# Kernel tuning notes

Hardware: AMD Instinct MI355X
Metric: run time of the kernel (lower is better)

The kernel has to match this reference:

```python
import jax, jax.numpy as jnp
import numpy as np

SHOT, WAY, DIM, Q, R = 5, 32, 640, 4096, 10
TEMP, L, DIV = 16.0, 2.0, 10.0
EPS = 1e-5


def _expmap0(x, c):
    # x: (..., d); c: broadcastable to (..., 1). Exponential map at origin + ball projection.
    sc = jnp.sqrt(c)
    n = jnp.maximum(jnp.linalg.norm(x, axis=-1, keepdims=True), EPS)
    y = jnp.tanh(sc * n) * x / (sc * n)
    ny = jnp.maximum(jnp.linalg.norm(y, axis=-1, keepdims=True), EPS)
    maxn = (1.0 - 1e-3) / sc
    return jnp.where(ny > maxn, y * (maxn / ny), y)


def _dist(x, y, c):
    # Poincare distance: 2/sqrt(c) * artanh(sqrt(c) * ||mobius_add(-x, y)||)
    u = -x
    uy = jnp.sum(u * y, -1, keepdims=True)
    u2 = jnp.sum(u * u, -1, keepdims=True)
    y2 = jnp.sum(y * y, -1, keepdims=True)
    num = (1.0 + 2.0 * c * uy + c * y2) * u + (1.0 - c * u2) * y
    den = jnp.maximum(1.0 + 2.0 * c * uy + c * c * u2 * y2, EPS)
    n = jnp.linalg.norm(num / den, axis=-1, keepdims=True)
    sc = jnp.sqrt(c)
    arg = jnp.clip(sc * n, 0.0, 1.0 - EPS)
    return ((2.0 / sc) * jnp.arctanh(arg))[..., 0]


def setup_inputs() -> dict:
    key = jax.random.key(0)
    ks = jax.random.split(key, 8)
    f = lambda k, s: jax.random.normal(k, s, dtype=jnp.float32)
    z = lambda s: jnp.zeros(s, jnp.float32)
    return {
        "data_shot": f(ks[0], (SHOT * WAY, DIM)),
        "data_query": f(ks[1], (Q, DIM)),
        "W1": f(ks[2], (2 * DIM, 128)) * 0.05, "b1": z((128,)),
        "W2": f(ks[3], (128, 64)) * 0.05, "b2": z((64,)),
        "W3": f(ks[4], (64, 5)) * 0.05, "b3": z((5,)),
        "Wr1": f(ks[5], (2 * R + 2, R)) * 0.05, "br1": z((R,)),
        "Wr2": f(ks[6], (R, R + 1)) * 0.05, "br2": z((R + 1,)),
    }


def reference(data_shot, data_query, W1, b1, W2, b2, W3, b3, Wr1, br1, Wr2, br2):
    # --- episode stats + per-class curvature controller ---
    all_data = jnp.concatenate([data_shot, data_query], 0).mean(0)      # (dim,)
    protos = data_shot.reshape(SHOT, WAY, DIM).mean(0)                  # (way, dim)
    ctrl_in = jnp.concatenate([protos, jnp.broadcast_to(all_data, (WAY, DIM))], 1)
    h = jax.nn.relu(ctrl_in @ W1 + b1)
    h = jax.nn.relu(h @ W2 + b2)
    cand = jnp.arange(1, 6, dtype=jnp.float32) * (L / DIV)              # 5 curvature candidates
    c = jax.nn.softmax(h @ W3 + b3, axis=-1) @ cand                     # (way,) positive curvature

    # --- hyperbolic projection + per-class proto-query distances (vectorized over classes) ---
    proto_p = _expmap0(protos, c[:, None])                              # (way, dim)
    query_p = _expmap0(data_query[None], c[:, None, None])              # (way, Q, dim)
    dis_mat = _dist(proto_p[:, None, :], query_p, c[:, None, None])     # (way, Q)

    # --- sort + gather-based rerank features ---
    idx = jnp.argsort(dis_mat, axis=1)
    idx_near, idx_far = idx[:, :R], idx[:, R:]
    n_i_d = jnp.take_along_axis(dis_mat, idx_near, 1)                   # (way, R)
    o_i_d = jnp.take_along_axis(dis_mat, idx_far, 1).mean(1)            # (way,)
    dT = dis_mat.T                                                      # (Q, way)
    Gnear = dT[idx_near]                                                # (way, R, way): [i,k,j] = dis_mat[j, idx_near[i,k]]
    n_o_d = (Gnear.sum(-1) - n_i_d) / (WAY - 1)                         # (way, R)
    Gfar = dT[idx_far]                                                  # (way, Q-R, way)
    ii = jnp.arange(WAY)
    mlt = (ii[None, :] < ii[:, None]).astype(dis_mat.dtype)             # j < i
    mgt = (ii[None, :] > ii[:, None]).astype(dis_mat.dtype)             # j > i
    sumA = jnp.einsum('ikj,ij->i', Gfar, mlt)                           # gathered cols (rows before i)
    sumB = mgt @ dis_mat[:, R:].sum(1)                                  # raw cols R: (rows after i, as in source)
    o_o_d = (sumA + sumB) / ((WAY - 1) * (Q - R))

    # --- rerank controller MLP ---
    rr_in = jnp.concatenate([n_i_d, n_o_d, o_i_d[:, None], o_o_d[:, None]], 1)  # (way, 2R+2)
    hr = jax.nn.relu(rr_in @ Wr1 + br1)
    orr = hr @ Wr2 + br2                                                # (way, R+1)
    i_w = jax.nn.softmax(orr[:, :R], axis=-1)                           # (way, R)
    onw = jax.nn.sigmoid(orr[:, R])                                     # (way,)

    # --- proto update + final distances ---
    near_q = data_query[idx_near]                                       # (way, R, dim)
    wdq = (near_q * i_w[:, :, None]).sum(1)                             # (way, dim)
    tmp = protos * onw[:, None] + wdq * (1.0 - onw[:, None])
    test_proto = _expmap0(tmp, c[:, None])
    new_dis = _dist(test_proto[:, None, :], query_p, c[:, None, None])  # (way, Q)
    return -new_dis.T / TEMP                                            # (Q, way)
```

## Files before the change

### kernel.cpp

```cpp
#include <hip/hip_runtime.h>
#include <math.h>

#define NSHOT 5
#define WAY 32
#define DIM 640
#define NQ 4096
#define RNEAR 10

constexpr int OFF_PROTOS = 0;
constexpr int OFF_QPART  = 20480;
constexpr int OFF_C      = 102400;
constexpr int OFF_BETA   = 102432;
constexpr int OFF_S      = 102464;
constexpr int OFF_U      = 102496;
constexpr int OFF_NID    = 102528;
constexpr int OFF_RR     = 102848;
constexpr int OFF_SPC    = 103552;
constexpr int OFF_H1P    = 103584;
constexpr int OFF_TP     = 107680;
constexpr int OFF_G      = 128160;
constexpr int OFF_NIDX   = 259232;
constexpr int OFF_Q2D    = 259556;
constexpr int OFF_X2D    = 267748;
constexpr int OFF_X2D2   = 267812;
constexpr int OFF_P2RAW  = 267876;

__device__ __forceinline__ double wave_sum_d(double v) {
#pragma unroll
  for (int o = 32; o > 0; o >>= 1) v += __shfl_down(v, o, 64);
  return v;
}

__device__ __forceinline__ double dist_hyp(double c, double xdotq, double u2, double q2) {
  const double EPSd = 1e-5;
  double sc = sqrt(c);
  double nq = sqrt(q2);
  double nf = fmax(nq, EPSd);
  double th = tanh(sc * nf);
  double al = th / (sc * nf);
  double ny = fmax(al * nq, EPSd);
  double mx = 0.999 / sc;
  if (ny > mx) al *= mx / ny;
  double y2 = al * al * q2;
  double uy = -al * xdotq;
  double A = 1.0 + 2.0 * c * uy + c * y2;
  double B = 1.0 - c * u2;
  double den = fmax(1.0 + 2.0 * c * uy + c * c * u2 * y2, EPSd);
  double num2 = fmax(A * A * u2 + 2.0 * A * B * uy + B * B * y2, 0.0);
  double n = sqrt(num2) / den;
  double arg = sc * n;
  const double CLIP = (double)(1.0f - 1e-5f);
  arg = fmin(fmax(arg, 0.0), CLIP);
  return (1.0 / sc) * log((1.0 + arg) / (1.0 - arg));
}

__device__ __forceinline__ float dist_f32(float c, float xdotq, float u2, float q2) {
  const float EPSf = 1e-5f;
  float sc = sqrtf(c);
  float nq = sqrtf(q2);
  float nf = fmaxf(nq, EPSf);
  float th = tanhf(sc * nf);
  float al = th / (sc * nf);
  float ny = fmaxf(al * nq, EPSf);
  float mx = 0.999f / sc;
  if (ny > mx) al *= mx / ny;
  float y2 = al * al * q2;
  float uy = -al * xdotq;
  float A = 1.f + 2.f * c * uy + c * y2;
  float B = 1.f - c * u2;
  float den = fmaxf(1.f + 2.f * c * uy + c * c * u2 * y2, EPSf);
  float num2 = fmaxf(A * A * u2 + 2.f * A * B * uy + B * B * y2, 0.f);
  float n = sqrtf(num2) / den;
  float arg = sc * n;
  arg = fminf(fmaxf(arg, 0.f), 1.f - 1e-5f);
  return (1.f / sc) * logf((1.f + arg) / (1.f - arg));
}

__device__ __forceinline__ double expmap_scale(double c, double p2, double* u2out) {
  double sc = sqrt(c);
  double ntrue = sqrt(p2);
  double nf = fmax(ntrue, 1e-5);
  double th = tanh(sc * nf);
  double s0 = th / (sc * nf);
  double ny = fmax(s0 * ntrue, 1e-5);
  double mx = 0.999 / sc;
  if (ny > mx) s0 *= mx / ny;
  *u2out = s0 * s0 * p2;
  return s0;
}

__global__ __launch_bounds__(640) void k_fuse1(const float* __restrict__ Qm,
                                               const float* __restrict__ shot,
                                               const float* __restrict__ W1, float* ws) {
  __shared__ double q2w[32][10];
  __shared__ double psred[10];
  __shared__ float pr[DIM];
  __shared__ float h1pp[5][128];
  int b = blockIdx.x, t = threadIdx.x;
  int lane = t & 63, wid = t >> 6;
  float protoval = 0.f;
  if (b < WAY) {
    float s = 0.f;
#pragma unroll
    for (int s5 = 0; s5 < NSHOT; ++s5) s += shot[(size_t)(s5 * WAY + b) * DIM + t];
    protoval = s * 0.2f;
    pr[t] = protoval;
    ws[OFF_PROTOS + b * DIM + t] = protoval;
    double pv2 = (double)protoval * protoval;
    pv2 = wave_sum_d(pv2);
    if (lane == 0) psred[wid] = pv2;
  }
  int r0 = b * 32;
  float colacc = 0.f;
  for (int r = 0; r < 32; ++r) {
    float v = Qm[(size_t)(r0 + r) * DIM + t];
    colacc += v;
    double sq = (double)v * v;
    sq = wave_sum_d(sq);
    if (lane == 0) q2w[r][wid] = sq;
  }
  ws[OFF_QPART + b * DIM + t] = colacc + 5.f * protoval;
  __syncthreads();
  if (t < 32) {
    double s = 0.0;
#pragma unroll
    for (int k = 0; k < 10; ++k) s += q2w[t][k];
    ((double*)(ws + OFF_Q2D))[r0 + t] = s;
  }
  if (b < WAY) {
    int n = t & 127, s = t >> 7;
    int k0 = s * 128;
    float acc = 0.f;
#pragma unroll 8
    for (int k = k0; k < k0 + 128; ++k) acc = fmaf(pr[k], W1[(size_t)k * 128 + n], acc);
    h1pp[s][n] = acc;
    __syncthreads();
    if (t < 128)
      ws[OFF_H1P + b * 128 + t] = h1pp[0][t] + h1pp[1][t] + h1pp[2][t] + h1pp[3][t] + h1pp[4][t];
    if (t == 0) {
      double p2 = 0.0;
#pragma unroll
      for (int k = 0; k < 10; ++k) p2 += psred[k];
      ((double*)(ws + OFF_P2RAW))[b] = p2;
    }
  }
}

__global__ __launch_bounds__(1024) void k_ctrl(const float* __restrict__ W1, const float* __restrict__ b1,
                                               const float* __restrict__ W2, const float* __restrict__ b2,
                                               const float* __restrict__ W3, const float* __restrict__ b3,
                                               float* ws) {
  __shared__ float am[DIM];
  __shared__ float part[8][128];
  __shared__ float part2[8][64];
  __shared__ float h1s[128], h2s[64], lg[5];
  int w = blockIdx.x, t = threadIdx.x;
  if (t < DIM) {
    const float* base = ws + OFF_QPART + t;
    float a0 = 0.f, a1 = 0.f, a2 = 0.f, a3 = 0.f;
#pragma unroll 8
    for (int p = 0; p < 128; p += 4) {
      a0 += base[(size_t)(p + 0) * DIM];
      a1 += base[(size_t)(p + 1) * DIM];
      a2 += base[(size_t)(p + 2) * DIM];
      a3 += base[(size_t)(p + 3) * DIM];
    }
    am[t] = ((a0 + a1) + (a2 + a3)) * (1.f / 4256.f);
  }
  __syncthreads();
  {
    int n = t & 127, s = t >> 7;
    int k0 = s * 80;
    float acc = 0.f;
#pragma unroll 8
    for (int k = k0; k < k0 + 80; ++k)
      acc = fmaf(am[k], W1[(size_t)(DIM + k) * 128 + n], acc);
    part[s][n] = acc;
  }
  __syncthreads();
  if (t < 128) {
    float a = ws[OFF_H1P + w * 128 + t] + b1[t];
#pragma unroll
    for (int s = 0; s < 8; ++s) a += part[s][t];
    h1s[t] = fmaxf(a, 0.f);
  }
  __syncthreads();
  if (t < 512) {
    int n = t & 63, s = t >> 6;
    int k0 = s * 16;
    float acc = 0.f;
#pragma unroll
    for (int k = 0; k < 16; ++k) acc = fmaf(h1s[k0 + k], W2[(size_t)(k0 + k) * 64 + n], acc);
    part2[s][n] = acc;
  }
  __syncthreads();
  if (t < 64) {
    float a = b2[t];
#pragma unroll
    for (int s = 0; s < 8; ++s) a += part2[s][t];
    h2s[t] = fmaxf(a, 0.f);
  }
  __syncthreads();
  if (t < 5) {
    float acc = b3[t];
    for (int k = 0; k < 64; ++k) acc = fmaf(h2s[k], W3[k * 5 + t], acc);
    lg[t] = acc;
  }
  __syncthreads();
  if (t == 0) {
    double m = lg[0];
    for (int i = 1; i < 5; ++i) m = fmax(m, (double)lg[i]);
    double se = 0.0, cv = 0.0;
    for (int i = 0; i < 5; ++i) { double e = exp((double)lg[i] - m); se += e; cv += e * 0.2 * (double)(i + 1); }
    double c = cv / se;
    ws[OFF_C + w] = (float)c;
    double p2 = ((const double*)(ws + OFF_P2RAW))[w];
    double u2;
    double beta = expmap_scale(c, p2, &u2);
    ws[OFF_BETA + w] = (float)beta;
    ((double*)(ws + OFF_X2D))[w] = u2;
  }
}

__global__ __launch_bounds__(256) void k_gemm(const float* __restrict__ X, const float* __restrict__ Qm,
                                              float* __restrict__ ws, int mode, float* __restrict__ out) {
  __shared__ float S[2][40][68];
  int t = threadIdx.x;
  int q0 = blockIdx.x * 8;
  int rowA = t >> 4, quadA = t & 15;
  int rowB = (t + 256) >> 4;
  int rowC = (t + 512) >> 4;
  bool hasC = (t < 128);
  const float* srcA = (rowA < 8 ? Qm + (size_t)(q0 + rowA) * DIM : X + (size_t)(rowA - 8) * DIM) + quadA * 4;
  const float* srcB = X + (size_t)(rowB - 8) * DIM + quadA * 4;
  const float* srcC = X + (size_t)(rowC - 8) * DIM + quadA * 4;
  float4 pA = *(const float4*)srcA;
  float4 pB = *(const float4*)srcB;
  float4 pC = {0.f, 0.f, 0.f, 0.f};
  if (hasC) pC = *(const float4*)srcC;
  *(float4*)&S[0][rowA][quadA * 4] = pA;
  *(float4*)&S[0][rowB][quadA * 4] = pB;
  if (hasC) *(float4*)&S[0][rowC][quadA * 4] = pC;
  __syncthreads();
  int q = t & 7, w = t >> 3;
  float ax = 0.f, ay = 0.f, az = 0.f, aw = 0.f;
  for (int c = 0; c < 10; ++c) {
    int bsel = c & 1;
    if (c < 9) {
      size_t kc = (size_t)(c + 1) * 64;
      pA = *(const float4*)(srcA + kc);
      pB = *(const float4*)(srcB + kc);
      if (hasC) pC = *(const float4*)(srcC + kc);
    }
    const float* qr = &S[bsel][q][0];
    const float* xr = &S[bsel][8 + w][0];
#pragma unroll
    for (int kk = 0; kk < 64; kk += 4) {
      float4 qv = *(const float4*)(qr + kk);
      float4 xv = *(const float4*)(xr + kk);
      ax = fmaf(qv.x, xv.x, ax);
      ay = fmaf(qv.y, xv.y, ay);
      az = fmaf(qv.z, xv.z, az);
      aw = fmaf(qv.w, xv.w, aw);
    }
    if (c < 9) {
      int nb = bsel ^ 1;
      *(float4*)&S[nb][rowA][quadA * 4] = pA;
      *(float4*)&S[nb][rowB][quadA * 4] = pB;
      if (hasC) *(float4*)&S[nb][rowC][quadA * 4] = pC;
      __syncthreads();
    }
  }
  float acc = (ax + ay) + (az + aw);
  int qq = q0 + q;
  const double* q2d = (const double*)(ws + OFF_Q2D);
  if (mode == 0) {
    const double* x2d = (const double*)(ws + OFF_X2D);
    float d = dist_f32(ws[OFF_C + w], ws[OFF_BETA + w] * acc, (float)x2d[w], (float)q2d[qq]);
    ws[OFF_G + (size_t)w * NQ + qq] = d;
  } else {
    const double* u2arr = (const double*)(ws + OFF_X2D2);
    double d = dist_hyp((double)ws[OFF_C + w], (double)acc, u2arr[w], q2d[qq]);
    out[(size_t)qq * WAY + w] = (float)(-d / 16.0);
  }
}

__global__ __launch_bounds__(1024) void k_topkA(float* __restrict__ ws) {
  __shared__ double sredS[16], sredU[16];
  __shared__ float cval[160];
  __shared__ int cidx[160];
  __shared__ float qvsh[RNEAR];
  __shared__ int qjsh[RNEAR];
  __shared__ float colsh[RNEAR][33];
  __shared__ float pcpart[RNEAR];
  int w = blockIdx.x, t = threadIdx.x;
  int lane = t & 63, wid = t >> 6;
  int* nidx = (int*)(ws + OFF_NIDX);
  const float* gb = ws + OFF_G + (size_t)w * NQ;
  float v0 = gb[t], v1 = gb[1024 + t], v2 = gb[2048 + t], v3 = gb[3072 + t];
  unsigned tk = 0;
  double s = (double)v0 + (double)v1 + (double)v2 + (double)v3;
  double u = (t < RNEAR) ? (double)v0 : 0.0;
  s = wave_sum_d(s);
  u = wave_sum_d(u);
  if (lane == 0) { sredS[wid] = s; sredU[wid] = u; }
  for (int r = 0; r < RNEAR; ++r) {
    float lv = INFINITY; int li = 0x7fffffff;
    if (!(tk & 1u) && (v0 < lv || (v0 == lv && t < li)))        { lv = v0; li = t; }
    if (!(tk & 2u) && (v1 < lv || (v1 == lv && 1024 + t < li))) { lv = v1; li = 1024 + t; }
    if (!(tk & 4u) && (v2 < lv || (v2 == lv && 2048 + t < li))) { lv = v2; li = 2048 + t; }
    if (!(tk & 8u) && (v3 < lv || (v3 == lv && 3072 + t < li))) { lv = v3; li = 3072 + t; }
#pragma unroll
    for (int o = 32; o > 0; o >>= 1) {
      float ov = __shfl_xor(lv, o, 64);
      int oi = __shfl_xor(li, o, 64);
      if (ov < lv || (ov == lv && oi < li)) { lv = ov; li = oi; }
    }
    if (lane == 0) { cval[wid * RNEAR + r] = lv; cidx[wid * RNEAR + r] = li; }
    if ((li & 1023) == t) tk |= 1u << (li >> 10);
  }
  __syncthreads();
  if (t == 0) {
    double S = 0.0, U = 0.0;
    for (int k = 0; k < 16; ++k) { S += sredS[k]; U += sredU[k]; }
    ws[OFF_S + w] = (float)S;
    ws[OFF_U + w] = (float)U;
  }
  if (t < 64) {
    float c0 = cval[t], c1 = cval[t + 64];
    int i0 = cidx[t], i1 = cidx[t + 64];
    float c2 = (t < 32) ? cval[t + 128] : INFINITY;
    int i2 = (t < 32) ? cidx[t + 128] : 0x7fffffff;
    unsigned m = 0;
    for (int r = 0; r < RNEAR; ++r) {
      float lv = INFINITY; int li = 0x7fffffff;
      if (!(m & 1u) && (c0 < lv || (c0 == lv && i0 < li))) { lv = c0; li = i0; }
      if (!(m & 2u) && (c1 < lv || (c1 == lv && i1 < li))) { lv = c1; li = i1; }
      if (!(m & 4u) && (c2 < lv || (c2 == lv && i2 < li))) { lv = c2; li = i2; }
#pragma unroll
      for (int o = 32; o > 0; o >>= 1) {
        float ov = __shfl_xor(lv, o, 64);
        int oi = __shfl_xor(li, o, 64);
        if (ov < lv || (ov == lv && oi < li)) { lv = ov; li = oi; }
      }
      if (lane == 0) { qvsh[r] = lv; qjsh[r] = li; }
      if (i0 == li) m |= 1u;
      if (i1 == li) m |= 2u;
      if (i2 == li) m |= 4u;
    }
  }
  __syncthreads();
  if (t < WAY * RNEAR) {
    int j = t >> 5, w2 = t & 31;
    colsh[j][w2] = ws[OFF_G + (size_t)w2 * NQ + qjsh[j]];
  }
  __syncthreads();
  if (t < RNEAR) {
    double cs = 0.0, pc = 0.0;
    for (int w2 = 0; w2 < WAY; ++w2) {
      float dv = colsh[t][w2];
      cs += dv;
      if (w2 < w) pc += dv;
    }
    ws[OFF_RR + w * 22 + t] = qvsh[t];
    ws[OFF_RR + w * 22 + RNEAR + t] = (float)((cs - qvsh[t]) / (double)(WAY - 1));
    ws[OFF_NID + w * RNEAR + t] = qvsh[t];
    nidx[w * RNEAR + t] = qjsh[t];
    pcpart[t] = (float)pc;
  }
  __syncthreads();
  if (t == 0) {
    double spc = 0.0, sn = 0.0;
    for (int j = 0; j < RNEAR; ++j) { spc += pcpart[j]; sn += qvsh[j]; }
    double S = (double)ws[OFF_S + w];
    ws[OFF_RR + w * 22 + 20] = (float)((S - sn) / (double)(NQ - RNEAR));
    ws[OFF_SPC + w] = (float)spc;
  }
}

__global__ __launch_bounds__(640) void k_refB(const float* __restrict__ Qm,
                                              const float* __restrict__ Wr1, const float* __restrict__ br1,
                                              const float* __restrict__ Wr2, const float* __restrict__ br2,
                                              float* __restrict__ ws) {
  __shared__ float Ssh[WAY], Ush[WAY];
  __shared__ float rrl[22];
  __shared__ int qj[RNEAR];
  __shared__ float hr[RNEAR], orsh[11], iw[RNEAR];
  __shared__ float onw_sh;
  __shared__ double p2red[10];
  __shared__ double gshd;
  int w = blockIdx.x, t = threadIdx.x;
  int lane = t & 63, wid = t >> 6;
  const int* nidx = (const int*)(ws + OFF_NIDX);
  if (t < WAY) { Ssh[t] = ws[OFF_S + t]; Ush[t] = ws[OFF_U + t]; }
  if (t >= 64 && t < 64 + 22) rrl[t - 64] = ws[OFF_RR + w * 22 + (t - 64)];
  if (t >= 96 && t < 96 + RNEAR) qj[t - 96] = nidx[w * RNEAR + (t - 96)];
  __syncthreads();
  if (t == 0) {
    double pref = 0.0, suf = 0.0;
    for (int j = 0; j < w; ++j) pref += (double)Ssh[j];
    for (int j = w + 1; j < WAY; ++j) suf += (double)Ssh[j] - (double)Ush[j];
    double spc = (double)ws[OFF_SPC + w];
    rrl[21] = (float)((pref - spc + suf) / ((double)(WAY - 1) * (double)(NQ - RNEAR)));
  }
  __syncthreads();
  if (t < RNEAR) {
    float a = br1[t];
    for (int k = 0; k < 22; ++k) a = fmaf(rrl[k], Wr1[k * RNEAR + t], a);
    hr[t] = fmaxf(a, 0.f);
  }
  __syncthreads();
  if (t < 11) {
    float a = br2[t];
    for (int k = 0; k < RNEAR; ++k) a = fmaf(hr[k], Wr2[k * 11 + t], a);
    orsh[t] = a;
  }
  __syncthreads();
  if (t == 0) {
    double m = orsh[0];
    for (int i = 1; i < RNEAR; ++i) m = fmax(m, (double)orsh[i]);
    double se = 0.0; double e[RNEAR];
    for (int i = 0; i < RNEAR; ++i) { e[i] = exp((double)orsh[i] - m); se += e[i]; }
    for (int i = 0; i < RNEAR; ++i) iw[i] = (float)(e[i] / se);
    onw_sh = (float)(1.0 / (1.0 + exp(-(double)orsh[10])));
  }
  __syncthreads();
  float onwv = onw_sh;
  float wd = 0.f;
#pragma unroll
  for (int j = 0; j < RNEAR; ++j)
    wd = fmaf(Qm[(size_t)qj[j] * DIM + t], iw[j], wd);
  float a0 = ws[OFF_PROTOS + w * DIM + t] * onwv + wd * (1.f - onwv);
  double ls = (double)a0 * a0;
  ls = wave_sum_d(ls);
  if (lane == 0) p2red[wid] = ls;
  __syncthreads();
  if (t == 0) {
    double p2 = 0.0;
#pragma unroll
    for (int k = 0; k < 10; ++k) p2 += p2red[k];
    double u22;
    gshd = expmap_scale((double)ws[OFF_C + w], p2, &u22);
    ((double*)(ws + OFF_X2D2))[w] = u22;
  }
  __syncthreads();
  ws[OFF_TP + w * DIM + t] = (float)gshd * a0;
}

extern "C" void kernel_launch(void* const* d_in, const int* in_sizes, int n_in,
                              void* d_out, int out_size, void* d_ws, size_t ws_size,
                              hipStream_t stream) {
  (void)in_sizes; (void)n_in; (void)out_size; (void)ws_size;
  const float* shot = (const float*)d_in[0];
  const float* qry  = (const float*)d_in[1];
  const float* W1   = (const float*)d_in[2];
  const float* b1   = (const float*)d_in[3];
  const float* W2   = (const float*)d_in[4];
  const float* b2   = (const float*)d_in[5];
  const float* W3   = (const float*)d_in[6];
  const float* b3   = (const float*)d_in[7];
  const float* Wr1  = (const float*)d_in[8];
  const float* br1  = (const float*)d_in[9];
  const float* Wr2  = (const float*)d_in[10];
  const float* br2  = (const float*)d_in[11];
  float* ws = (float*)d_ws;
  float* out = (float*)d_out;

  hipLaunchKernelGGL(k_fuse1, dim3(128), dim3(640), 0, stream, qry, shot, W1, ws);
  hipLaunchKernelGGL(k_ctrl,  dim3(32), dim3(1024), 0, stream, W1, b1, W2, b2, W3, b3, ws);
  hipLaunchKernelGGL(k_gemm,  dim3(512), dim3(256), 0, stream, ws + OFF_PROTOS, qry, ws, 0, out);
  hipLaunchKernelGGL(k_topkA, dim3(32), dim3(1024), 0, stream, ws);
  hipLaunchKernelGGL(k_refB,  dim3(32), dim3(640), 0, stream, qry, Wr1, br1, Wr2, br2, ws);
  hipLaunchKernelGGL(k_gemm,  dim3(512), dim3(256), 0, stream, ws + OFF_TP, qry, ws, 1, out);
}
```

Before: 85.18 us.

## Split controller kernel to compute shared all-data mean and W1 half once

The old controller kernel had every one of 32 class blocks redundantly reduce the 128 query partial sums into the global mean and multiply it by the lower half of W1. That work is now done once in a new 8-block kernel, where each block handles an 80-wide slice and writes a partial h1 contribution. A slimmer 128-thread per-class kernel then sums those partials and runs the small remaining MLP layers. This removes redundant loads and FLOPs but adds one extra kernel launch and a small global-memory round trip.

```diff
diff --git a/kernel.cpp b/kernel.cpp
--- a/kernel.cpp
+++ b/kernel.cpp
@@ -24,6 +24,7 @@
 constexpr int OFF_X2D    = 267748;
 constexpr int OFF_X2D2   = 267812;
 constexpr int OFF_P2RAW  = 267876;
+constexpr int OFF_H1PART = 268000;
 
 __device__ __forceinline__ double wave_sum_d(double v) {
 #pragma unroll
@@ -146,60 +147,68 @@
   }
 }
 
-__global__ __launch_bounds__(1024) void k_ctrl(const float* __restrict__ W1, const float* __restrict__ b1,
+__global__ __launch_bounds__(320) void k_amw1(const float* __restrict__ W1, float* ws) {
+  __shared__ float part_am[4][80];
+  __shared__ float am_s[80];
+  __shared__ float h1part[2][128];
+  int j = blockIdx.x, t = threadIdx.x;
+  {
+    int c = t % 80, pg = t / 80;
+    const float* base = ws + OFF_QPART + j * 80 + c;
+    int p0 = pg * 32;
+    float a0 = 0.f, a1 = 0.f, a2 = 0.f, a3 = 0.f;
+#pragma unroll 8
+    for (int p = 0; p < 32; p += 4) {
+      a0 += base[(size_t)(p0 + p + 0) * DIM];
+      a1 += base[(size_t)(p0 + p + 1) * DIM];
+      a2 += base[(size_t)(p0 + p + 2) * DIM];
+      a3 += base[(size_t)(p0 + p + 3) * DIM];
+    }
+    part_am[pg][c] = (a0 + a1) + (a2 + a3);
+  }
+  __syncthreads();
+  if (t < 80)
+    am_s[t] = (part_am[0][t] + part_am[1][t] + part_am[2][t] + part_am[3][t]) * (1.f / 4256.f);
+  __syncthreads();
+  if (t < 256) {
+    int n = t & 127, kh = t >> 7;
+    int kbase = j * 80 + kh * 40;
+    float acc = 0.f;
+#pragma unroll 8
+    for (int k = 0; k < 40; ++k)
+      acc = fmaf(am_s[kh * 40 + k], W1[(size_t)(DIM + kbase + k) * 128 + n], acc);
+    h1part[kh][n] = acc;
+  }
+  __syncthreads();
+  if (t < 128) ws[OFF_H1PART + j * 128 + t] = h1part[0][t] + h1part[1][t];
+}
+
+__global__ __launch_bounds__(128) void k_ctrl2(const float* __restrict__ b1,
                                                const float* __restrict__ W2, const float* __restrict__ b2,
                                                const float* __restrict__ W3, const float* __restrict__ b3,
                                                float* ws) {
-  __shared__ float am[DIM];
-  __shared__ float part[8][128];
-  __shared__ float part2[8][64];
-  __shared__ float h1s[128], h2s[64], lg[5];
+  __shared__ float h1s[128];
+  __shared__ float h2p[2][64];
+  __shared__ float h2s[64], lg[5];
   int w = blockIdx.x, t = threadIdx.x;
-  if (t < DIM) {
-    const float* base = ws + OFF_QPART + t;
-    float a0 = 0.f, a1 = 0.f, a2 = 0.f, a3 = 0.f;
-#pragma unroll 8
-    for (int p = 0; p < 128; p += 4) {
-      a0 += base[(size_t)(p + 0) * DIM];
-      a1 += base[(size_t)(p + 1) * DIM];
-      a2 += base[(size_t)(p + 2) * DIM];
-      a3 += base[(size_t)(p + 3) * DIM];
-    }
-    am[t] = ((a0 + a1) + (a2 + a3)) * (1.f / 4256.f);
-  }
-  __syncthreads();
   {
-    int n = t & 127, s = t >> 7;
-    int k0 = s * 80;
+    float a = ws[OFF_H1P + w * 128 + t] + b1[t];
+#pragma unroll
+    for (int j = 0; j < 8; ++j) a += ws[OFF_H1PART + j * 128 + t];
+    h1s[t] = fmaxf(a, 0.f);
+  }
+  __syncthreads();
+  {
+    int n = t & 63, kh = t >> 6;
+    int k0 = kh * 64;
     float acc = 0.f;
 #pragma unroll 8
-    for (int k = k0; k < k0 + 80; ++k)
-      acc = fmaf(am[k], W1[(size_t)(DIM + k) * 128 + n], acc);
-    part[s][n] = acc;
-  }
-  __syncthreads();
-  if (t < 128) {
-    float a = ws[OFF_H1P + w * 128 + t] + b1[t];
-#pragma unroll
-    for (int s = 0; s < 8; ++s) a += part[s][t];
-    h1s[t] = fmaxf(a, 0.f);
-  }
-  __syncthreads();
-  if (t < 512) {
-    int n = t & 63, s = t >> 6;
-    int k0 = s * 16;
-    float acc = 0.f;
-#pragma unroll
-    for (int k = 0; k < 16; ++k) acc = fmaf(h1s[k0 + k], W2[(size_t)(k0 + k) * 64 + n], acc);
-    part2[s][n] = acc;
-  }
-  __syncthreads();
-  if (t < 64) {
-    float a = b2[t];
-#pragma unroll
-    for (int s = 0; s < 8; ++s) a += part2[s][t];
-    h2s[t] = fmaxf(a, 0.f);
-  }
+    for (int k = 0; k < 64; ++k)
+      acc = fmaf(h1s[k0 + k], W2[(size_t)(k0 + k) * 64 + n], acc);
+    h2p[kh][n] = acc;
+  }
+  __syncthreads();
+  if (t < 64) h2s[t] = fmaxf(h2p[0][t] + h2p[1][t] + b2[t], 0.f);
   __syncthreads();
   if (t < 5) {
     float acc = b3[t];
@@ -467,7 +476,8 @@
   float* out = (float*)d_out;
 
   hipLaunchKernelGGL(k_fuse1, dim3(128), dim3(640), 0, stream, qry, shot, W1, ws);
-  hipLaunchKernelGGL(k_ctrl,  dim3(32), dim3(1024), 0, stream, W1, b1, W2, b2, W3, b3, ws);
+  hipLaunchKernelGGL(k_amw1,  dim3(8), dim3(320), 0, stream, W1, ws);
+  hipLaunchKernelGGL(k_ctrl2, dim3(32), dim3(128), 0, stream, b1, W2, b2, W3, b3, ws);
   hipLaunchKernelGGL(k_gemm,  dim3(512), dim3(256), 0, stream, ws + OFF_PROTOS, qry, ws, 0, out);
   hipLaunchKernelGGL(k_topkA, dim3(32), dim3(1024), 0, stream, ws);
   hipLaunchKernelGGL(k_refB,  dim3(32), dim3(640), 0, stream, qry, Wr1, br1, Wr2, br2, ws);
```

After: 81.65 us. 1.04x faster.
